# Performance work log

Hardware: AMD Instinct MI355X
Metric: run time of the kernel (lower is better)

The kernel has to match this reference:

```python
import jax, jax.numpy as jnp
import numpy as np

B, D, LC, LQ = 64, 256, 1024, 128
P_DROP = 0.1


def setup_inputs() -> dict:
    key = jax.random.key(0)
    k1, k2, k3 = jax.random.split(key, 3)
    C = jax.random.normal(k1, (B, D, LC), dtype=jnp.float32)
    Q = jax.random.normal(k2, (B, D, LQ), dtype=jnp.float32)
    # xavier_normal_ on [B, 1, 3D]: std = sqrt(2 / (fan_in + fan_out)) = sqrt(2 / (1 + 3D))
    std = (2.0 / (1.0 + 3.0 * D)) ** 0.5
    W = jax.random.normal(k3, (B, 1, 3 * D), dtype=jnp.float32) * std
    return {"C": C, "Q": Q, "W": W}


def reference(C, Q, W):
    # Trilinear similarity, algebraically decomposed:
    # S[b,i,j] = W . cat([Q[:,:,j], C[:,:,i], Q[:,:,j]*C[:,:,i]])
    wq, wc, wm = jnp.split(W[:, 0, :], 3, axis=1)          # each [B, D]
    sq = jnp.einsum('bd,bdj->bj', wq, Q)                    # [B, LQ]
    sc = jnp.einsum('bd,bdi->bi', wc, C)                    # [B, LC]
    sm = jnp.einsum('bd,bdi,bdj->bij', wm, C, Q)            # [B, LC, LQ]
    S = sm + sc[:, :, None] + sq[:, None, :]                # [B, LC, LQ]

    S_ = jax.nn.softmax(S, axis=2)    # row softmax over question positions
    S__ = jax.nn.softmax(S, axis=1)   # column softmax over context positions

    # A = Q @ S_^T : [B, D, LC]
    A = jnp.einsum('bdj,bij->bdi', Q, S_)
    # Bmat = C @ (S_ @ S__^T)^T : first M = S__^T-contracted C, then with S_
    M = jnp.einsum('bdk,bkj->bdj', C, S__)                  # [B, D, LQ]
    Bmat = jnp.einsum('bdj,bij->bdi', M, S_)                # [B, D, LC]

    out = jnp.concatenate([C, A, C * A, C * Bmat], axis=1)  # [B, 4D, LC]

    # F.dropout(p, training=True) with a fixed key (deterministic reference)
    keep = jax.random.bernoulli(jax.random.key(42), 1.0 - P_DROP, out.shape)
    return jnp.where(keep, out / (1.0 - P_DROP), 0.0)
```

## Files before the change

kernel.cpp:

```cpp
#include <hip/hip_runtime.h>
#include <stdint.h>
#include <stddef.h>

#define NB  64
#define ND  256
#define NLC 1024
#define NLQ 128
#define INVKEEP (1.0f/0.9f)

#define OFF_SQ    0u
#define OFF_U     8192u
#define OFF_V     139264u
#define OFF_COLP  155648u
#define OFF_SBT   286720u
#define OFF_SBF   8544256u
#define OFF_M     12738560u
#define OFF_QB    13787136u

typedef float f32x4  __attribute__((ext_vector_type(4)));
typedef short bf16x8 __attribute__((ext_vector_type(8)));

__device__ __forceinline__ uint32_t f2bf(float x) {
  const uint32_t u = __float_as_uint(x);
  return (u + 0x7fffu + ((u >> 16) & 1u)) >> 16;
}
__device__ __forceinline__ uint32_t cvtpk(float lo, float hi) {
  uint32_t r;
  asm("v_cvt_pk_bf16_f32 %0, %1, %2" : "=v"(r) : "v"(lo), "v"(hi));
  return r;
}

__device__ __forceinline__ void tf_round(uint32_t& a, uint32_t& b, const int r) {
  a += b;
  b = (b << r) | (b >> (32 - r));
  b ^= a;
}
__device__ __forceinline__ uint32_t threefry_xor(uint32_t x0, uint32_t x1) {
  const uint32_t ks0 = 0u, ks1 = 42u, ks2 = 0x1BD11BDAu ^ 0u ^ 42u;
  x0 += ks0; x1 += ks1;
  tf_round(x0,x1,13); tf_round(x0,x1,15); tf_round(x0,x1,26); tf_round(x0,x1,6);
  x0 += ks1; x1 += ks2 + 1u;
  tf_round(x0,x1,17); tf_round(x0,x1,29); tf_round(x0,x1,16); tf_round(x0,x1,24);
  x0 += ks2; x1 += ks0 + 2u;
  tf_round(x0,x1,13); tf_round(x0,x1,15); tf_round(x0,x1,26); tf_round(x0,x1,6);
  x0 += ks0; x1 += ks1 + 3u;
  tf_round(x0,x1,17); tf_round(x0,x1,29); tf_round(x0,x1,16); tf_round(x0,x1,24);
  x0 += ks1; x1 += ks2 + 4u;
  tf_round(x0,x1,13); tf_round(x0,x1,15); tf_round(x0,x1,26); tf_round(x0,x1,6);
  x0 += ks2; x1 += ks0 + 5u;
  return x0 ^ x1;
}

__global__ __launch_bounds__(128) void k_sq(const float* __restrict__ Q,
                                            const float* __restrict__ W,
                                            float* __restrict__ ws) {
  const int b = blockIdx.x;
  const int j = threadIdx.x;
  const float* wq = W + (size_t)b*768;
  const float* Qb = Q + (size_t)b*ND*NLQ;
  float acc = 0.0f;
  for (int d = 0; d < ND; ++d) acc = fmaf(wq[d], Qb[(size_t)d*NLQ + j], acc);
  ws[OFF_SQ + (size_t)b*NLQ + j] = acc;
}

__global__ __launch_bounds__(256) void k_qb(const float* __restrict__ Q,
                                            float* __restrict__ ws) {
  const size_t idx = ((size_t)blockIdx.x * 256 + threadIdx.x) * 8;
  ushort* qb = (ushort*)(ws + OFF_QB);
  const float4 a = *(const float4*)&Q[idx];
  const float4 c = *(const float4*)&Q[idx + 4];
  uint4 pk;
  pk.x = cvtpk(a.x, a.y); pk.y = cvtpk(a.z, a.w);
  pk.z = cvtpk(c.x, c.y); pk.w = cvtpk(c.z, c.w);
  *(uint4*)&qb[idx] = pk;
}

__global__ __launch_bounds__(256) void k_s(const float* __restrict__ C,
                                           const float* __restrict__ Q,
                                           const float* __restrict__ W,
                                           float* __restrict__ ws) {
  __shared__ __align__(16) uint8_t smem[40960];
  float (*Cs)[129] = (float(*)[129])smem;
  float (*Qs)[129] = (float(*)[129])(smem + 16512);
  float* wmS = (float*)(smem + 33024);
  float* wcS = (float*)(smem + 34048);
  float* sqS = (float*)(smem + 35072);
  ushort (*T)[128]   = (ushort(*)[128])smem;
  float  (*colm)[128] = (float(*)[128])(smem + 35584);
  float  (*cols)[128] = (float(*)[128])(smem + 37632);

  const int n  = blockIdx.x;
  const int rr = n & 7, qq = n >> 3;
  const int it = qq & 7;
  const int b  = (qq >> 3) * 8 + rr;
  const int i0 = it * 128;
  const int t  = threadIdx.x;
  wcS[t] = W[(size_t)b*768 + 256 + t];
  wmS[t] = W[(size_t)b*768 + 512 + t];
  if (t < 128) sqS[t] = ws[OFF_SQ + (size_t)b*NLQ + t];

  const float* Cb = C + (size_t)b*ND*NLC;
  const float* Qb = Q + (size_t)b*ND*NLQ;
  const int l  = t & 63, w = t >> 6;
  const int lm = l & 15, lg = l >> 4;

  f32x4 acc[2][8];
  #pragma unroll
  for (int mg = 0; mg < 2; ++mg)
    #pragma unroll
    for (int nf = 0; nf < 8; ++nf) acc[mg][nf] = (f32x4)0.0f;

  for (int d0 = 0; d0 < ND; d0 += 32) {
    __syncthreads();
    #pragma unroll
    for (int p = 0; p < 4; ++p) {
      const int f  = p*256 + t;
      const int dk = f >> 5, x4 = f & 31;
      *(float4*)&Cs[dk][x4*4] = *(const float4*)&Cb[(size_t)(d0+dk)*NLC + i0 + x4*4];
      const float4 qv = *(const float4*)&Qb[(size_t)(d0+dk)*NLQ + x4*4];
      const float wmv = wmS[d0+dk], wcv = wcS[d0+dk];
      float4 o;
      o.x = fmaf(wmv, qv.x, wcv);
      o.y = fmaf(wmv, qv.y, wcv);
      o.z = fmaf(wmv, qv.z, wcv);
      o.w = fmaf(wmv, qv.w, wcv);
      *(float4*)&Qs[dk][x4*4] = o;
    }
    __syncthreads();
    bf16x8 bq[8];
    #pragma unroll
    for (int nf = 0; nf < 8; ++nf) {
      const int j = nf*16 + lm;
      union { uint32_t u[4]; bf16x8 v; } cc;
      #pragma unroll
      for (int kk = 0; kk < 4; ++kk)
        cc.u[kk] = cvtpk(Qs[lg*8 + kk*2][j], Qs[lg*8 + kk*2 + 1][j]);
      bq[nf] = cc.v;
    }
    #pragma unroll
    for (int mg = 0; mg < 2; ++mg) {
      const int i = w*32 + mg*16 + lm;
      union { uint32_t u[4]; bf16x8 v; } ca;
      #pragma unroll
      for (int kk = 0; kk < 4; ++kk)
        ca.u[kk] = cvtpk(Cs[lg*8 + kk*2][i], Cs[lg*8 + kk*2 + 1][i]);
      #pragma unroll
      for (int nf = 0; nf < 8; ++nf)
        acc[mg][nf] = __builtin_amdgcn_mfma_f32_16x16x32_bf16(ca.v, bq[nf], acc[mg][nf], 0, 0, 0);
    }
  }

  float sqv[8];
  #pragma unroll
  for (int nf = 0; nf < 8; ++nf) sqv[nf] = sqS[nf*16 + lm];
  __syncthreads();

  #pragma unroll
  for (int mg = 0; mg < 2; ++mg) {
    #pragma unroll
    for (int r = 0; r < 4; ++r) {
      const int row = w*32 + mg*16 + lg*4 + r;
      float sv[8], e[8];
      #pragma unroll
      for (int nf = 0; nf < 8; ++nf) sv[nf] = acc[mg][nf][r] + sqv[nf];
      float mx = sv[0];
      #pragma unroll
      for (int nf = 1; nf < 8; ++nf) mx = fmaxf(mx, sv[nf]);
      mx = fmaxf(mx, __shfl_xor(mx, 1));
      mx = fmaxf(mx, __shfl_xor(mx, 2));
      mx = fmaxf(mx, __shfl_xor(mx, 4));
      mx = fmaxf(mx, __shfl_xor(mx, 8));
      float sm = 0.0f;
      #pragma unroll
      for (int nf = 0; nf < 8; ++nf) { e[nf] = __expf(sv[nf] - mx); sm += e[nf]; }
      sm += __shfl_xor(sm, 1); sm += __shfl_xor(sm, 2);
      sm += __shfl_xor(sm, 4); sm += __shfl_xor(sm, 8);
      const float ir = 1.0f / sm;
      const int po = ((row & 7) ^ ((row >> 3) & 7)) << 3;
      #pragma unroll
      for (int nf = 0; nf < 8; ++nf)
        T[row][(nf*16 + lm) ^ po] = (ushort)f2bf(e[nf] * ir);
      if (lm == 0) ws[OFF_U + (size_t)b*NLC + i0 + row] = __expf(mx) * sm;
    }
  }

  float cmx[8];
  #pragma unroll
  for (int nf = 0; nf < 8; ++nf) {
    float m2 = -3.0e38f;
    #pragma unroll
    for (int mg = 0; mg < 2; ++mg)
      #pragma unroll
      for (int r = 0; r < 4; ++r)
        m2 = fmaxf(m2, acc[mg][nf][r] + sqv[nf]);
    m2 = fmaxf(m2, __shfl_xor(m2, 16));
    m2 = fmaxf(m2, __shfl_xor(m2, 32));
    cmx[nf] = m2;
  }
  if (lg == 0) {
    #pragma unroll
    for (int nf = 0; nf < 8; ++nf) colm[w][nf*16 + lm] = cmx[nf];
  }
  __syncthreads();
  #pragma unroll
  for (int nf = 0; nf < 8; ++nf) {
    const int j = nf*16 + lm;
    const float cmb = fmaxf(fmaxf(colm[0][j], colm[1][j]),
                            fmaxf(colm[2][j], colm[3][j]));
    float cs = 0.0f;
    #pragma unroll
    for (int mg = 0; mg < 2; ++mg)
      #pragma unroll
      for (int r = 0; r < 4; ++r)
        cs += __expf(acc[mg][nf][r] + sqv[nf] - cmb);
    cs += __shfl_xor(cs, 16);
    cs += __shfl_xor(cs, 32);
    if (lg == 0) cols[w][j] = cs;
  }
  __syncthreads();

  ushort* Sb16 = (ushort*)(ws + OFF_SBF) + ((size_t)b*NLC + (size_t)i0)*NLQ;
  #pragma unroll
  for (int p = 0; p < 8; ++p) {
    const int f = p*256 + t;
    const int i = f >> 4, jo = f & 15;
    const int po = ((i & 7) ^ ((i >> 3) & 7)) << 3;
    *(uint4*)&Sb16[(size_t)i*NLQ + jo*8] = *(const uint4*)&T[i][(jo*8) ^ po];
  }
  ushort* SBTg = (ushort*)(ws + OFF_SBT) + (size_t)b*NLQ*NLC + i0;
  #pragma unroll
  for (int p = 0; p < 8; ++p) {
    const int f = p*256 + t;
    const int j = f >> 4, io = f & 15;
    uint32_t wd4[4];
    #pragma unroll
    for (int h = 0; h < 4; ++h) {
      const uint32_t v0 = T[io*8 + h*2    ][j ^ (((h*2    ) ^ (io & 7)) << 3)];
      const uint32_t v1 = T[io*8 + h*2 + 1][j ^ (((h*2 + 1) ^ (io & 7)) << 3)];
      wd4[h] = v0 | (v1 << 16);
    }
    *(uint4*)&SBTg[(size_t)j*NLC + io*8] = *(uint4*)wd4;
  }
  if (t < 128) {
    const float cm = fmaxf(fmaxf(colm[0][t], colm[1][t]),
                           fmaxf(colm[2][t], colm[3][t]));
    const float s  = cols[0][t] + cols[1][t] + cols[2][t] + cols[3][t];
    float2* cp = (float2*)(ws + OFF_COLP) + ((size_t)b*8 + it)*128 + t;
    *cp = make_float2(cm, s);
  }
}

__global__ __launch_bounds__(128) void k_cred(float* __restrict__ ws) {
  const int b = blockIdx.x, j = threadIdx.x;
  const float2* cp = (const float2*)(ws + OFF_COLP) + (size_t)b*8*128 + j;
  float m = -3.0e38f, s = 0.0f;
  #pragma unroll
  for (int it = 0; it < 8; ++it) {
    const float2 p = cp[(size_t)it*128];
    const float nm = fmaxf(m, p.x);
    s = s * __expf(m - nm) + p.y * __expf(p.x - nm);
    m = nm;
  }
  ws[OFF_V + (size_t)b*NLQ + j] = __expf(-m) / s;
}

__global__ __launch_bounds__(256) void k_m(const float* __restrict__ C,
                                           float* __restrict__ ws) {
  __shared__ ushort Cp[32][40];
  __shared__ ushort Ts[128][40];
  __shared__ float u_l[1024];
  __shared__ float v_l[128];
  const int n  = blockIdx.x;
  const int rr = n & 7, qq = n >> 3;
  const int dq = qq & 7;
  const int b  = (qq >> 3) * 8 + rr;
  const int t  = threadIdx.x;
  const int l  = t & 63, w = t >> 6;
  const int wd = w & 1, wj = w >> 1;
  const int lm = l & 15, lg = l >> 4;
  for (int kk = t; kk < 1024; kk += 256) u_l[kk] = ws[OFF_U + (size_t)b*NLC + kk];
  if (t < 128) v_l[t] = ws[OFF_V + (size_t)b*NLQ + t];

  f32x4 acc[4];
  #pragma unroll
  for (int nf = 0; nf < 4; ++nf) acc[nf] = (f32x4)0.0f;

  const float*  Cb   = C + (size_t)b*ND*NLC + (size_t)dq*32*NLC;
  const ushort* SBTg = (const ushort*)(ws + OFF_SBT) + (size_t)b*NLQ*NLC;

  for (int kt = 0; kt < 32; ++kt) {
    const int k0 = kt*32;
    __syncthreads();
    {
      const int dl = t >> 3, kq = t & 7;
      const float4 cv = *(const float4*)&Cb[(size_t)dl*NLC + k0 + kq*4];
      const int kb = k0 + kq*4;
      uint2 pk;
      pk.x = cvtpk(cv.x * u_l[kb+0], cv.y * u_l[kb+1]);
      pk.y = cvtpk(cv.z * u_l[kb+2], cv.w * u_l[kb+3]);
      *(uint2*)&Cp[dl][kq*4] = pk;
    }
    #pragma unroll
    for (int p = 0; p < 2; ++p) {
      const int f = p*256 + t;
      const int jr = f >> 2, k8 = (f & 3)*8;
      *(uint4*)&Ts[jr][k8] = *(const uint4*)&SBTg[(size_t)jr*NLC + k0 + k8];
    }
    __syncthreads();
    union { uint32_t u[4]; bf16x8 v; } ca;
    *(uint4*)ca.u = *(const uint4*)&Cp[wd*16 + lm][lg*8];
    #pragma unroll
    for (int nf = 0; nf < 4; ++nf) {
      union { uint32_t u[4]; bf16x8 v; } cb;
      *(uint4*)cb.u = *(const uint4*)&Ts[wj*64 + nf*16 + lm][lg*8];
      acc[nf] = __builtin_amdgcn_mfma_f32_16x16x32_bf16(ca.v, cb.v, acc[nf], 0, 0, 0);
    }
  }
  ushort* Mp = (ushort*)(ws + OFF_M) + (size_t)b*ND*NLQ + (size_t)dq*32*NLQ;
  #pragma unroll
  for (int nf = 0; nf < 4; ++nf) {
    const int j = wj*64 + nf*16 + lm;
    const float vj = v_l[j];
    #pragma unroll
    for (int r = 0; r < 4; ++r) {
      const int d = wd*16 + lg*4 + r;
      Mp[(size_t)d*NLQ + j] = (ushort)f2bf(acc[nf][r] * vj);
    }
  }
}

__global__ __launch_bounds__(256, 4) void k_final(const float* __restrict__ C,
                                                  float* __restrict__ ws,
                                                  float* __restrict__ out) {
  __shared__ __align__(16) uint8_t smem[40960];
  ushort (*St)[128] = (ushort(*)[128])smem;
  ushort (*Qt)[128] = (ushort(*)[128])(smem + 32768);
  ushort (*Mt)[128] = (ushort(*)[128])(smem + 36864);
  float  (*At)[128] = (float (*)[128])smem;
  float  (*Bt)[128] = (float (*)[128])(smem + 8192);

  const int n  = blockIdx.x;
  const int r8 = n & 7, q = n >> 3;
  const int m  = q & 15;
  const int g  = (q >> 4) * 8 + r8;
  const int b  = g & 63;
  const int i0 = (g >> 6) * 128;
  const int d0 = m * 16;
  const int t  = threadIdx.x;

  const ushort* Sp = (const ushort*)(ws + OFF_SBF) + ((size_t)b*NLC + i0)*NLQ;
  #pragma unroll
  for (int p = 0; p < 8; ++p) {
    const int f  = p*256 + t;
    const int jo = f & 15;
    const int il = f >> 4;
    *(uint4*)&St[il][(jo*8) ^ ((il & 7) << 3)] =
        *(const uint4*)&Sp[(size_t)il*NLQ + jo*8];
  }
  const ushort* Qp = (const ushort*)(ws + OFF_QB) + (size_t)b*ND*NLQ + (size_t)d0*NLQ;
  const ushort* Mp = (const ushort*)(ws + OFF_M)  + (size_t)b*ND*NLQ + (size_t)d0*NLQ;
  {
    const int jo = t & 15;
    const int dl = t >> 4;
    const int col = (jo*8) ^ ((dl & 7) << 3);
    *(uint4*)&Qt[dl][col] = *(const uint4*)&Qp[(size_t)dl*NLQ + jo*8];
    *(uint4*)&Mt[dl][col] = *(const uint4*)&Mp[(size_t)dl*NLQ + jo*8];
  }
  __syncthreads();

  const int w  = t >> 6;
  const int l  = t & 63;
  const int lm = l & 15;
  const int lk = (l >> 4) * 8;
  const int sw = (lm & 7) << 3;

  f32x4 accA[2], accB[2];
  #pragma unroll
  for (int f = 0; f < 2; ++f) { accA[f] = (f32x4)0.0f; accB[f] = (f32x4)0.0f; }

  #pragma unroll
  for (int ks = 0; ks < 4; ++ks) {
    const int koff = (ks*32 + lk) ^ sw;
    const bf16x8 qf = *(const bf16x8*)&Qt[lm][koff];
    const bf16x8 mf = *(const bf16x8*)&Mt[lm][koff];
    #pragma unroll
    for (int f = 0; f < 2; ++f) {
      const bf16x8 sf = *(const bf16x8*)&St[(w*2 + f)*16 + lm][koff];
      accA[f] = __builtin_amdgcn_mfma_f32_16x16x32_bf16(qf, sf, accA[f], 0, 0, 0);
      accB[f] = __builtin_amdgcn_mfma_f32_16x16x32_bf16(mf, sf, accB[f], 0, 0, 0);
    }
  }
  __syncthreads();

  const int dwl = (l >> 4) * 4;
  #pragma unroll
  for (int f = 0; f < 2; ++f) {
    const int i = (w*2 + f)*16 + lm;
    #pragma unroll
    for (int r = 0; r < 4; ++r) {
      const int dl = dwl + r;
      const int isw = i ^ ((dl & 7) << 2);
      At[dl][isw] = accA[f][r];
      Bt[dl][isw] = accB[f][r];
    }
  }
  __syncthreads();

  const int il4 = (t & 31) * 4;
  const int dg8 = t >> 5;
  const float* Cb = C + (size_t)b*ND*NLC;
  #pragma unroll 1
  for (int dd = 0; dd < 2; ++dd) {
    const int dl = dd*8 + dg8;
    const int d  = d0 + dl;
    const int isw = il4 ^ ((dl & 7) << 2);
    const float4 a4 = *(const float4*)&At[dl][isw];
    const float4 b4 = *(const float4*)&Bt[dl][isw];
    const float4 c4 = *(const float4*)&Cb[(size_t)d*NLC + i0 + il4];
    const float av[4] = {a4.x, a4.y, a4.z, a4.w};
    const float bv[4] = {b4.x, b4.y, b4.z, b4.w};
    const float cv[4] = {c4.x, c4.y, c4.z, c4.w};
    #pragma unroll
    for (int s = 0; s < 4; ++s) {
      const uint32_t nb = ((((uint32_t)b << 10) + (uint32_t)(s*ND + d)) << 10)
                          + (uint32_t)(i0 + il4);
      float ov[4];
      #pragma unroll
      for (int e = 0; e < 4; ++e) {
        const uint32_t bits = threefry_xor(0u, nb + (uint32_t)e);
        float v;
        if (s == 0)      v = cv[e];
        else if (s == 1) v = av[e];
        else if (s == 2) v = cv[e] * av[e];
        else             v = cv[e] * bv[e];
        ov[e] = ((bits >> 9) < 7549747u) ? v * INVKEEP : 0.0f;
      }
      *(float4*)&out[nb] = make_float4(ov[0], ov[1], ov[2], ov[3]);
    }
  }
}

extern "C" void kernel_launch(void* const* d_in, const int* in_sizes, int n_in,
                              void* d_out, int out_size, void* d_ws, size_t ws_size,
                              hipStream_t stream) {
  (void)in_sizes; (void)n_in; (void)out_size; (void)ws_size;
  const float* C = (const float*)d_in[0];
  const float* Q = (const float*)d_in[1];
  const float* W = (const float*)d_in[2];
  float* out = (float*)d_out;
  float* ws  = (float*)d_ws;

  hipLaunchKernelGGL(k_sq,    dim3(NB),   dim3(128), 0, stream, Q, W, ws);
  hipLaunchKernelGGL(k_qb,    dim3(1024), dim3(256), 0, stream, Q, ws);
  hipLaunchKernelGGL(k_s,     dim3(512),  dim3(256), 0, stream, C, Q, W, ws);
  hipLaunchKernelGGL(k_cred,  dim3(NB),   dim3(128), 0, stream, ws);
  hipLaunchKernelGGL(k_m,     dim3(512),  dim3(256), 0, stream, C, ws);
  hipLaunchKernelGGL(k_final, dim3(8192), dim3(256), 0, stream, C, ws, out);
}
```

Measured before the change: 217.4 us.

## Fuse Q preprocessing into one prep kernel and deepen k_m K tile

Merges the sq reduction and the bf16 Q conversion into a single k_prep kernel. That kernel also precomputes a transposed bf16 copy of wm*Q+wc, so k_s loads ready-made MFMA operands instead of recomputing and converting Q in every tile. k_m now uses a 64-wide K step, which halves its loop iterations and barriers at the cost of larger LDS tiles. The dropout threshold compare is also simplified to an equivalent single unsigned compare.

```diff
diff --git a/kernel.cpp b/kernel.cpp
--- a/kernel.cpp
+++ b/kernel.cpp
@@ -8,11 +8,12 @@
 #define NLQ 128
 #define INVKEEP (1.0f/0.9f)
 
-#define OFF_SQ    0u
-#define OFF_U     8192u
-#define OFF_V     139264u
-#define OFF_COLP  155648u
-#define OFF_SBT   286720u
+#define OFF_SQP   0u
+#define OFF_U     32768u
+#define OFF_V     98304u
+#define OFF_COLP  106496u
+#define OFF_SBT   237568u
+#define OFF_QT    4431872u
 #define OFF_SBF   8544256u
 #define OFF_M     12738560u
 #define OFF_QB    13787136u
@@ -51,43 +52,74 @@
   return x0 ^ x1;
 }
 
-__global__ __launch_bounds__(128) void k_sq(const float* __restrict__ Q,
-                                            const float* __restrict__ W,
-                                            float* __restrict__ ws) {
-  const int b = blockIdx.x;
-  const int j = threadIdx.x;
-  const float* wq = W + (size_t)b*768;
+__global__ __launch_bounds__(256) void k_prep(const float* __restrict__ Q,
+                                              const float* __restrict__ W,
+                                              float* __restrict__ ws) {
+  __shared__ __align__(16) float Qs[64][129];
+  __shared__ float wqS[64], wmS[64], wcS[64];
+  __shared__ float red[8][128];
+  const int n = blockIdx.x;
+  const int b = n >> 2, c = n & 3;
+  const int d0 = c * 64;
+  const int t = threadIdx.x;
+  if (t < 64) {
+    wqS[t] = W[(size_t)b*768 + d0 + t];
+    wcS[t] = W[(size_t)b*768 + 256 + d0 + t];
+    wmS[t] = W[(size_t)b*768 + 512 + d0 + t];
+  }
+  __syncthreads();
   const float* Qb = Q + (size_t)b*ND*NLQ;
-  float acc = 0.0f;
-  for (int d = 0; d < ND; ++d) acc = fmaf(wq[d], Qb[(size_t)d*NLQ + j], acc);
-  ws[OFF_SQ + (size_t)b*NLQ + j] = acc;
-}
-
-__global__ __launch_bounds__(256) void k_qb(const float* __restrict__ Q,
-                                            float* __restrict__ ws) {
-  const size_t idx = ((size_t)blockIdx.x * 256 + threadIdx.x) * 8;
-  ushort* qb = (ushort*)(ws + OFF_QB);
-  const float4 a = *(const float4*)&Q[idx];
-  const float4 c = *(const float4*)&Q[idx + 4];
-  uint4 pk;
-  pk.x = cvtpk(a.x, a.y); pk.y = cvtpk(a.z, a.w);
-  pk.z = cvtpk(c.x, c.y); pk.w = cvtpk(c.z, c.w);
-  *(uint4*)&qb[idx] = pk;
+  ushort* QBg = (ushort*)(ws + OFF_QB) + (size_t)b*ND*NLQ;
+  const int j4 = t & 31, y = t >> 5;
+  float sq4[4] = {0.0f, 0.0f, 0.0f, 0.0f};
+  #pragma unroll
+  for (int p = 0; p < 8; ++p) {
+    const int dk = p*8 + y;
+    const float4 qv = *(const float4*)&Qb[(size_t)(d0+dk)*NLQ + j4*4];
+    *(float4*)&Qs[dk][j4*4] = qv;
+    uint2 pk;
+    pk.x = cvtpk(qv.x, qv.y);
+    pk.y = cvtpk(qv.z, qv.w);
+    *(uint2*)&QBg[(size_t)(d0+dk)*NLQ + j4*4] = pk;
+    const float wq = wqS[dk];
+    sq4[0] = fmaf(wq, qv.x, sq4[0]);
+    sq4[1] = fmaf(wq, qv.y, sq4[1]);
+    sq4[2] = fmaf(wq, qv.z, sq4[2]);
+    sq4[3] = fmaf(wq, qv.w, sq4[3]);
+  }
+  #pragma unroll
+  for (int e = 0; e < 4; ++e) red[y][j4*4 + e] = sq4[e];
+  __syncthreads();
+  const int j = t >> 1, dh = (t & 1) * 32;
+  uint32_t pk16[16];
+  #pragma unroll
+  for (int kk = 0; kk < 32; kk += 2) {
+    const float q0 = fmaf(wmS[dh+kk],   Qs[dh+kk][j],   wcS[dh+kk]);
+    const float q1 = fmaf(wmS[dh+kk+1], Qs[dh+kk+1][j], wcS[dh+kk+1]);
+    pk16[kk >> 1] = cvtpk(q0, q1);
+  }
+  ushort* QTg = (ushort*)(ws + OFF_QT) + (size_t)b*NLQ*ND + (size_t)j*ND + d0 + dh;
+  *(uint4*)&QTg[0]  = *(uint4*)&pk16[0];
+  *(uint4*)&QTg[8]  = *(uint4*)&pk16[4];
+  *(uint4*)&QTg[16] = *(uint4*)&pk16[8];
+  *(uint4*)&QTg[24] = *(uint4*)&pk16[12];
+  if (t < 128) {
+    float s = 0.0f;
+    #pragma unroll
+    for (int yy = 0; yy < 8; ++yy) s += red[yy][t];
+    ws[OFF_SQP + ((size_t)b*4 + c)*128 + t] = s;
+  }
 }
 
 __global__ __launch_bounds__(256) void k_s(const float* __restrict__ C,
-                                           const float* __restrict__ Q,
-                                           const float* __restrict__ W,
                                            float* __restrict__ ws) {
-  __shared__ __align__(16) uint8_t smem[40960];
-  float (*Cs)[129] = (float(*)[129])smem;
-  float (*Qs)[129] = (float(*)[129])(smem + 16512);
-  float* wmS = (float*)(smem + 33024);
-  float* wcS = (float*)(smem + 34048);
-  float* sqS = (float*)(smem + 35072);
-  ushort (*T)[128]   = (ushort(*)[128])smem;
-  float  (*colm)[128] = (float(*)[128])(smem + 35584);
-  float  (*cols)[128] = (float(*)[128])(smem + 37632);
+  __shared__ __align__(16) uint8_t smem[37376];
+  float  (*Cs)[129] = (float(*)[129])smem;
+  ushort (*Qt)[40]  = (ushort(*)[40])(smem + 16512);
+  ushort (*T)[128]  = (ushort(*)[128])smem;
+  float*  sqS       = (float*)(smem + 32768);
+  float  (*colm)[128] = (float(*)[128])(smem + 33280);
+  float  (*cols)[128] = (float(*)[128])(smem + 35328);
 
   const int n  = blockIdx.x;
   const int rr = n & 7, qq = n >> 3;
@@ -95,12 +127,13 @@
   const int b  = (qq >> 3) * 8 + rr;
   const int i0 = it * 128;
   const int t  = threadIdx.x;
-  wcS[t] = W[(size_t)b*768 + 256 + t];
-  wmS[t] = W[(size_t)b*768 + 512 + t];
-  if (t < 128) sqS[t] = ws[OFF_SQ + (size_t)b*NLQ + t];
-
-  const float* Cb = C + (size_t)b*ND*NLC;
-  const float* Qb = Q + (size_t)b*ND*NLQ;
+  if (t < 128) {
+    const float* sp = ws + OFF_SQP + (size_t)b*4*128 + t;
+    sqS[t] = sp[0] + sp[128] + sp[256] + sp[384];
+  }
+
+  const float*  Cb  = C + (size_t)b*ND*NLC;
+  const ushort* QTg = (const ushort*)(ws + OFF_QT) + (size_t)b*NLQ*ND;
   const int l  = t & 63, w = t >> 6;
   const int lm = l & 15, lg = l >> 4;
 
@@ -117,26 +150,18 @@
       const int f  = p*256 + t;
       const int dk = f >> 5, x4 = f & 31;
       *(float4*)&Cs[dk][x4*4] = *(const float4*)&Cb[(size_t)(d0+dk)*NLC + i0 + x4*4];
-      const float4 qv = *(const float4*)&Qb[(size_t)(d0+dk)*NLQ + x4*4];
-      const float wmv = wmS[d0+dk], wcv = wcS[d0+dk];
-      float4 o;
-      o.x = fmaf(wmv, qv.x, wcv);
-      o.y = fmaf(wmv, qv.y, wcv);
-      o.z = fmaf(wmv, qv.z, wcv);
-      o.w = fmaf(wmv, qv.w, wcv);
-      *(float4*)&Qs[dk][x4*4] = o;
+    }
+    #pragma unroll
+    for (int p = 0; p < 2; ++p) {
+      const int f  = p*256 + t;
+      const int jr = f >> 2, k8 = (f & 3)*8;
+      *(uint4*)&Qt[jr][k8] = *(const uint4*)&QTg[(size_t)jr*ND + d0 + k8];
     }
     __syncthreads();
     bf16x8 bq[8];
     #pragma unroll
-    for (int nf = 0; nf < 8; ++nf) {
-      const int j = nf*16 + lm;
-      union { uint32_t u[4]; bf16x8 v; } cc;
-      #pragma unroll
-      for (int kk = 0; kk < 4; ++kk)
-        cc.u[kk] = cvtpk(Qs[lg*8 + kk*2][j], Qs[lg*8 + kk*2 + 1][j]);
-      bq[nf] = cc.v;
-    }
+    for (int nf = 0; nf < 8; ++nf)
+      bq[nf] = *(const bf16x8*)&Qt[nf*16 + lm][lg*8];
     #pragma unroll
     for (int mg = 0; mg < 2; ++mg) {
       const int i = w*32 + mg*16 + lm;
@@ -266,8 +291,8 @@
 
 __global__ __launch_bounds__(256) void k_m(const float* __restrict__ C,
                                            float* __restrict__ ws) {
-  __shared__ ushort Cp[32][40];
-  __shared__ ushort Ts[128][40];
+  __shared__ ushort Cp[32][72];
+  __shared__ ushort Ts[128][72];
   __shared__ float u_l[1024];
   __shared__ float v_l[128];
   const int n  = blockIdx.x;
@@ -288,32 +313,38 @@
   const float*  Cb   = C + (size_t)b*ND*NLC + (size_t)dq*32*NLC;
   const ushort* SBTg = (const ushort*)(ws + OFF_SBT) + (size_t)b*NLQ*NLC;
 
-  for (int kt = 0; kt < 32; ++kt) {
-    const int k0 = kt*32;
+  for (int kt = 0; kt < 16; ++kt) {
+    const int k0 = kt*64;
     __syncthreads();
     {
       const int dl = t >> 3, kq = t & 7;
-      const float4 cv = *(const float4*)&Cb[(size_t)dl*NLC + k0 + kq*4];
-      const int kb = k0 + kq*4;
-      uint2 pk;
-      pk.x = cvtpk(cv.x * u_l[kb+0], cv.y * u_l[kb+1]);
-      pk.y = cvtpk(cv.z * u_l[kb+2], cv.w * u_l[kb+3]);
-      *(uint2*)&Cp[dl][kq*4] = pk;
-    }
-    #pragma unroll
-    for (int p = 0; p < 2; ++p) {
+      const float4 c0 = *(const float4*)&Cb[(size_t)dl*NLC + k0 + kq*8];
+      const float4 c1 = *(const float4*)&Cb[(size_t)dl*NLC + k0 + kq*8 + 4];
+      const int kb = k0 + kq*8;
+      uint4 pk;
+      pk.x = cvtpk(c0.x * u_l[kb+0], c0.y * u_l[kb+1]);
+      pk.y = cvtpk(c0.z * u_l[kb+2], c0.w * u_l[kb+3]);
+      pk.z = cvtpk(c1.x * u_l[kb+4], c1.y * u_l[kb+5]);
+      pk.w = cvtpk(c1.z * u_l[kb+6], c1.w * u_l[kb+7]);
+      *(uint4*)&Cp[dl][kq*8] = pk;
+    }
+    #pragma unroll
+    for (int p = 0; p < 4; ++p) {
       const int f = p*256 + t;
-      const int jr = f >> 2, k8 = (f & 3)*8;
+      const int jr = f >> 3, k8 = (f & 7)*8;
       *(uint4*)&Ts[jr][k8] = *(const uint4*)&SBTg[(size_t)jr*NLC + k0 + k8];
     }
     __syncthreads();
-    union { uint32_t u[4]; bf16x8 v; } ca;
-    *(uint4*)ca.u = *(const uint4*)&Cp[wd*16 + lm][lg*8];
-    #pragma unroll
-    for (int nf = 0; nf < 4; ++nf) {
-      union { uint32_t u[4]; bf16x8 v; } cb;
-      *(uint4*)cb.u = *(const uint4*)&Ts[wj*64 + nf*16 + lm][lg*8];
-      acc[nf] = __builtin_amdgcn_mfma_f32_16x16x32_bf16(ca.v, cb.v, acc[nf], 0, 0, 0);
+    #pragma unroll
+    for (int ks = 0; ks < 2; ++ks) {
+      union { uint32_t u[4]; bf16x8 v; } ca;
+      *(uint4*)ca.u = *(const uint4*)&Cp[wd*16 + lm][ks*32 + lg*8];
+      #pragma unroll
+      for (int nf = 0; nf < 4; ++nf) {
+        union { uint32_t u[4]; bf16x8 v; } cb;
+        *(uint4*)cb.u = *(const uint4*)&Ts[wj*64 + nf*16 + lm][ks*32 + lg*8];
+        acc[nf] = __builtin_amdgcn_mfma_f32_16x16x32_bf16(ca.v, cb.v, acc[nf], 0, 0, 0);
+      }
     }
   }
   ushort* Mp = (ushort*)(ws + OFF_M) + (size_t)b*ND*NLQ + (size_t)dq*32*NLQ;
@@ -433,7 +464,7 @@
         else if (s == 1) v = av[e];
         else if (s == 2) v = cv[e] * av[e];
         else             v = cv[e] * bv[e];
-        ov[e] = ((bits >> 9) < 7549747u) ? v * INVKEEP : 0.0f;
+        ov[e] = (bits < 3865470464u) ? v * INVKEEP : 0.0f;
       }
       *(float4*)&out[nb] = make_float4(ov[0], ov[1], ov[2], ov[3]);
     }
@@ -450,9 +481,8 @@
   float* out = (float*)d_out;
   float* ws  = (float*)d_ws;
 
-  hipLaunchKernelGGL(k_sq,    dim3(NB),   dim3(128), 0, stream, Q, W, ws);
-  hipLaunchKernelGGL(k_qb,    dim3(1024), dim3(256), 0, stream, Q, ws);
-  hipLaunchKernelGGL(k_s,     dim3(512),  dim3(256), 0, stream, C, Q, W, ws);
+  hipLaunchKernelGGL(k_prep,  dim3(256),  dim3(256), 0, stream, Q, W, ws);
+  hipLaunchKernelGGL(k_s,     dim3(512),  dim3(256), 0, stream, C, ws);
   hipLaunchKernelGGL(k_cred,  dim3(NB),   dim3(128), 0, stream, ws);
   hipLaunchKernelGGL(k_m,     dim3(512),  dim3(256), 0, stream, C, ws);
   hipLaunchKernelGGL(k_final, dim3(8192), dim3(256), 0, stream, C, ws, out);
```

Result: faster. 182.0 us (-16.3%).
